# Optimization experiments

Hardware: AMD Instinct MI355X
Metric: run time of the kernel (lower is better)

The kernel has to match this reference:

```python
import jax, jax.numpy as jnp
import numpy as np

DIM = 64
TIME_DIM = 16
LABEL_DIM = 32
N_HEADS = 4
B = 524288


def _mha(seq, w_in, b_in, w_out, b_out, n_heads=N_HEADS):
    # seq: [B, S, E]; faithful nn.MultiheadAttention (batch_first) self-attention
    Bs, S, E = seq.shape
    D = E // n_heads
    qkv = seq @ w_in + b_in  # [B, S, 3E]
    q, k, v = jnp.split(qkv, 3, axis=-1)
    q = q.reshape(Bs, S, n_heads, D)
    k = k.reshape(Bs, S, n_heads, D)
    v = v.reshape(Bs, S, n_heads, D)
    scale = 1.0 / jnp.sqrt(jnp.asarray(D, seq.dtype))
    scores = jnp.einsum('bshd,bthd->bhst', q, k) * scale
    attn = jax.nn.softmax(scores, axis=-1)
    o = jnp.einsum('bhst,bthd->bshd', attn, v).reshape(Bs, S, E)
    return o @ w_out + b_out


def setup_inputs() -> dict:
    key = jax.random.key(0)
    ks = iter(jax.random.split(key, 64))

    def p(shape):
        return jax.random.normal(next(ks), shape, dtype=jnp.float32) * 0.05

    inp = {
        'x': jax.random.normal(next(ks), (B, DIM), dtype=jnp.float32),
        't': jax.random.uniform(next(ks), (B, 1), dtype=jnp.float32),
        'y': jax.random.normal(next(ks), (B, 40), dtype=jnp.float32),
        # label_proj: Linear(40,32) -> ReLU -> Linear(32,64)
        'lp_w1': p((40, LABEL_DIM)), 'lp_b1': p((LABEL_DIM,)),
        'lp_w2': p((LABEL_DIM, DIM)), 'lp_b2': p((DIM,)),
        # two MultiheadAttention layers (packed in_proj, out_proj)
        'a1_win': p((DIM, 3 * DIM)), 'a1_bin': p((3 * DIM,)),
        'a1_wout': p((DIM, DIM)), 'a1_bout': p((DIM,)),
        'a2_win': p((DIM, 3 * DIM)), 'a2_bin': p((3 * DIM,)),
        'a2_wout': p((DIM, DIM)), 'a2_bout': p((DIM,)),
        # FiLM layers: gamma/beta Linear(dim, dim)
        'f1_gw': p((DIM, DIM)), 'f1_gb': p((DIM,)),
        'f1_bw': p((DIM, DIM)), 'f1_bb': p((DIM,)),
        'f2_gw': p((DIM, DIM)), 'f2_gb': p((DIM,)),
        'f2_bw': p((DIM, DIM)), 'f2_bb': p((DIM,)),
        # block1: Linear(80,64)->ReLU->Linear(64,64); block2/3: Linear(64,64)x2
        'b1_w1': p((DIM + TIME_DIM, DIM)), 'b1_b1': p((DIM,)),
        'b1_w2': p((DIM, DIM)), 'b1_b2': p((DIM,)),
        'b2_w1': p((DIM, DIM)), 'b2_b1': p((DIM,)),
        'b2_w2': p((DIM, DIM)), 'b2_b2': p((DIM,)),
        'b3_w1': p((DIM, DIM)), 'b3_b1': p((DIM,)),
        'b3_w2': p((DIM, DIM)), 'b3_b2': p((DIM,)),
        'out_w': p((DIM, DIM)), 'out_b': p((DIM,)),
    }
    return inp


def reference(x, t, y,
              lp_w1, lp_b1, lp_w2, lp_b2,
              a1_win, a1_bin, a1_wout, a1_bout,
              a2_win, a2_bin, a2_wout, a2_bout,
              f1_gw, f1_gb, f1_bw, f1_bb,
              f2_gw, f2_gb, f2_bw, f2_bb,
              b1_w1, b1_b1, b1_w2, b1_b2,
              b2_w1, b2_b1, b2_w2, b2_b2,
              b3_w1, b3_b1, b3_w2, b3_b2,
              out_w, out_b):
    half = TIME_DIM // 2
    freq = (2.0 ** jnp.arange(half, dtype=x.dtype)) * jnp.pi  # [8]
    args = t * freq[None, :]                                   # [B, 8]
    t_feats = jnp.concatenate([jnp.sin(args), jnp.cos(args)], axis=-1)  # [B, 16]

    h = jnp.concatenate([x, t_feats], axis=-1)                 # [B, 80]
    h = jax.nn.relu(h @ b1_w1 + b1_b1) @ b1_w2 + b1_b2         # block1

    y_embed = jax.nn.relu(y @ lp_w1 + lp_b1) @ lp_w2 + lp_b2   # [B, 64]

    seq = jnp.stack([h, y_embed], axis=1)                      # [B, 2, 64]
    h = _mha(seq, a1_win, a1_bin, a1_wout, a1_bout)[:, 0]
    h = (y_embed @ f1_gw + f1_gb) * h + (y_embed @ f1_bw + f1_bb)  # FiLM1
    h = h + (jax.nn.relu(h @ b2_w1 + b2_b1) @ b2_w2 + b2_b2)   # block2 + residual

    seq = jnp.stack([h, y_embed], axis=1)
    h = _mha(seq, a2_win, a2_bin, a2_wout, a2_bout)[:, 0]
    h = (y_embed @ f2_gw + f2_gb) * h + (y_embed @ f2_bw + f2_bb)  # FiLM2
    h = h + (jax.nn.relu(h @ b3_w1 + b3_b1) @ b3_w2 + b3_b2)   # block3 + residual

    return h @ out_w + out_b
```

## Files before the change

kernel.cpp:

```cpp
#include <hip/hip_runtime.h>
#include <math.h>

typedef __attribute__((ext_vector_type(8))) short   short8;
typedef __attribute__((ext_vector_type(8))) _Float16 half8;
typedef __attribute__((ext_vector_type(2))) __fp16  fp16x2;
typedef __attribute__((ext_vector_type(4))) float   f32x4;

__device__ __forceinline__ half8 as_h8(short8 s) {
  union { short8 s; half8 h; } u; u.s = s; return u.h;
}
#define MFMA16(a,b,c) __builtin_amdgcn_mfma_f32_16x16x32_f16(as_h8(a), as_h8(b), (c), 0, 0, 0)

#define WS_B1W1   0
#define WS_B1W2   12
#define WS_LPW1   20
#define WS_LPW2   24
#define WS_A1WIN  28
#define WS_A1WOUT 52
#define WS_F1GW   60
#define WS_F1BW   68
#define WS_B2W1   76
#define WS_B2W2   84
#define WS_A2WIN  92
#define WS_A2WOUT 116
#define WS_F2GW   124
#define WS_F2BW   132
#define WS_B3W1   140
#define WS_B3W2   148
#define WS_OUTW   156
#define WS_FRAGS  164

__device__ __forceinline__ unsigned short f2h(float f) {
  union { _Float16 h; unsigned short u; } r;
  r.h = (_Float16)f;
  return r.u;
}
__device__ __forceinline__ unsigned int pkrtz(float lo, float hi) {
  union { fp16x2 h; unsigned int u; } r;
  r.h = __builtin_amdgcn_cvt_pkrtz(lo, hi);
  return r.u;
}
__device__ __forceinline__ float h_lo(unsigned int p) {
  union { unsigned short s; _Float16 h; } c; c.s = (unsigned short)p; return (float)c.h;
}
__device__ __forceinline__ float h_hi(unsigned int p) {
  union { unsigned short s; _Float16 h; } c; c.s = (unsigned short)(p >> 16); return (float)c.h;
}

__device__ __forceinline__ short8 pack8(float4 a, float4 b) {
  union { unsigned int u[4]; short8 s; } r;
  r.u[0] = pkrtz(a.x, a.y);
  r.u[1] = pkrtz(a.z, a.w);
  r.u[2] = pkrtz(b.x, b.y);
  r.u[3] = pkrtz(b.z, b.w);
  return r.s;
}

__device__ __forceinline__ short8 zero8() {
  short8 r;
  #pragma unroll
  for (int j = 0; j < 8; ++j) r[j] = 0;
  return r;
}

__device__ __forceinline__ short8 neg8(short8 a) {
  union { short8 s; unsigned int u[4]; } r;
  r.s = a;
  #pragma unroll
  for (int i = 0; i < 4; ++i) r.u[i] ^= 0x80008000u;
  return r.s;
}

__device__ __forceinline__ f32x4 relu4(f32x4 v) {
  f32x4 r;
  #pragma unroll
  for (int j = 0; j < 4; ++j) r[j] = fmaxf(v[j], 0.0f);
  return r;
}

__global__ __launch_bounds__(64) void prep_kernel(
    const float* b1w1, const float* b1w2, const float* lpw1, const float* lpw2,
    const float* a1win, const float* a1wout, const float* f1gw, const float* f1bw,
    const float* b2w1, const float* b2w2, const float* a2win, const float* a2wout,
    const float* f2gw, const float* f2bw, const float* b3w1, const float* b3w2,
    const float* outw, unsigned short* ws)
{
  const float* WS_[17] = {b1w1,b1w2,lpw1,lpw2,a1win,a1wout,f1gw,f1bw,b2w1,b2w2,
                          a2win,a2wout,f2gw,f2bw,b3w1,b3w2,outw};
  const int KA[17] = {80,64,40,32,64,64,64,64,64,64,64,64,64,64,64,64,64};
  const int NA[17] = {64,64,32,64,192,64,64,64,64,64,192,64,64,64,64,64,64};
  const int FO[17] = {0,12,20,24,28,52,60,68,76,84,92,116,124,132,140,148,156};

  const int b = blockIdx.x;
  int m = 0;
  #pragma unroll
  for (int i = 1; i < 17; ++i) if (b >= FO[i]) m = i;
  const int f  = b - FO[m];
  const int K  = KA[m], N = NA[m];
  const int kc = (K + 31) >> 5;
  const int n  = f / kc, c = f % kc;

  const int lane = threadIdx.x;
  const int col  = n * 16 + (lane & 15);
  const int kb   = c * 32 + ((lane >> 4) * 8);
  const float* W = WS_[m];

  short8 r;
  #pragma unroll
  for (int j = 0; j < 8; ++j) {
    const int k = kb + j;
    const float v = (k < K) ? W[(size_t)k * N + col] : 0.0f;
    r[j] = (short)f2h(v);
  }
  *reinterpret_cast<short8*>(ws + (size_t)b * 512 + lane * 8) = r;
}

__device__ __forceinline__ short8 ldA(const unsigned short* Ab, int c) {
  return *reinterpret_cast<const short8*>(Ab + c * 32);
}
__device__ __forceinline__ void stC_pk(unsigned short* Cb, int n, unsigned int p01, unsigned int p23) {
  unsigned short* p = Cb + n * 16;
  p[0]   = (unsigned short)p01;
  p[72]  = (unsigned short)(p01 >> 16);
  p[144] = (unsigned short)p23;
  p[216] = (unsigned short)(p23 >> 16);
}
__device__ __forceinline__ void stC(unsigned short* Cb, int n, f32x4 v) {
  stC_pk(Cb, n, pkrtz(v[0], v[1]), pkrtz(v[2], v[3]));
}
__device__ __forceinline__ float rowsum16(float v) {
  float r = v;
  r += __int_as_float(__builtin_amdgcn_update_dpp(
        __float_as_int(r), __float_as_int(r), 0x128, 0xf, 0xf, false));
  r += __int_as_float(__builtin_amdgcn_update_dpp(
        __float_as_int(r), __float_as_int(r), 0x124, 0xf, 0xf, false));
  r += __int_as_float(__builtin_amdgcn_update_dpp(
        __float_as_int(r), __float_as_int(r), 0x122, 0xf, 0xf, false));
  r += __int_as_float(__builtin_amdgcn_update_dpp(
        __float_as_int(r), __float_as_int(r), 0x121, 0xf, 0xf, false));
  return r;
}

__global__ __launch_bounds__(256, 4) void flow_mfma(
    const float* __restrict__ x, const float* __restrict__ t, const float* __restrict__ y,
    const float* __restrict__ b1b1, const float* __restrict__ b1b2,
    const float* __restrict__ lpb1, const float* __restrict__ lpb2,
    const float* __restrict__ a1bin, const float* __restrict__ a1bout,
    const float* __restrict__ f1gb, const float* __restrict__ f1bb,
    const float* __restrict__ b2b1, const float* __restrict__ b2b2,
    const float* __restrict__ a2bin, const float* __restrict__ a2bout,
    const float* __restrict__ f2gb, const float* __restrict__ f2bb,
    const float* __restrict__ b3b1, const float* __restrict__ b3b2,
    const float* __restrict__ outb,
    const unsigned short* __restrict__ ws,
    float* __restrict__ out, int Btotal)
{
  __shared__ __align__(16) unsigned short lds[4][2 * 16 * 72];
  const int tid  = threadIdx.x;
  const int lane = tid & 63, wid = tid >> 6;
  const int lrow = lane & 15, grp = lane >> 4;
  const int r0   = (blockIdx.x * 4 + wid) * 32;
  if (r0 >= Btotal) return;
  unsigned short* T = &lds[wid][0];
  unsigned short* Ab[2];
  unsigned short* Cb[2];
  #pragma unroll
  for (int u = 0; u < 2; ++u) {
    Ab[u] = T + u * 1152 + lrow * 72 + grp * 8;
    Cb[u] = T + u * 1152 + grp * 288 + lrow;
  }
  const short8* wsl = reinterpret_cast<const short8*>(ws) + lane;

  short8 hA0[2], hA1[2];
  {
    short8 tF[2];
    #pragma unroll
    for (int u = 0; u < 2; ++u) {
      const size_t row = (size_t)r0 + u * 16 + lrow;
      const float4* xp = reinterpret_cast<const float4*>(x + row * 64) + grp * 2;
      hA0[u] = pack8(xp[0], xp[1]);
      hA1[u] = pack8(xp[8], xp[9]);
      const float tv = t[row];
      float s = sinf(3.14159265358979323846f * tv);
      float c = cosf(3.14159265358979323846f * tv);
      short8 hp;
      #pragma unroll
      for (int j = 0; j < 8; ++j) {
        const float v = (grp == 0) ? s : ((grp == 1) ? c : 0.0f);
        hp[j] = (short)f2h(v);
        const float s2 = 2.0f * s * c;
        const float c2 = 1.0f - 2.0f * s * s;
        s = s2; c = c2;
      }
      tF[u] = hp;
    }
    #pragma unroll
    for (int n = 0; n < 4; ++n) {
      const short8 B0 = wsl[(WS_B1W1 + n * 3 + 0) * 64];
      const short8 B1 = wsl[(WS_B1W1 + n * 3 + 1) * 64];
      const short8 B2 = wsl[(WS_B1W1 + n * 3 + 2) * 64];
      const float bias = b1b1[n * 16 + lrow];
      #pragma unroll
      for (int u = 0; u < 2; ++u) {
        f32x4 acc = {bias, bias, bias, bias};
        acc = MFMA16(hA0[u], B0, acc);
        acc = MFMA16(hA1[u], B1, acc);
        acc = MFMA16(tF[u],  B2, acc);
        stC(Cb[u], n, relu4(acc));
      }
    }
  }
  #pragma unroll
  for (int u = 0; u < 2; ++u) { hA0[u] = ldA(Ab[u], 0); hA1[u] = ldA(Ab[u], 1); }
  #pragma unroll
  for (int n = 0; n < 4; ++n) {
    const short8 B0 = wsl[(WS_B1W2 + n * 2 + 0) * 64];
    const short8 B1 = wsl[(WS_B1W2 + n * 2 + 1) * 64];
    const float bias = b1b2[n * 16 + lrow];
    #pragma unroll
    for (int u = 0; u < 2; ++u) {
      f32x4 acc = {bias, bias, bias, bias};
      acc = MFMA16(hA0[u], B0, acc);
      acc = MFMA16(hA1[u], B1, acc);
      stC(Cb[u], n, acc);
    }
  }
  #pragma unroll
  for (int u = 0; u < 2; ++u) { hA0[u] = ldA(Ab[u], 0); hA1[u] = ldA(Ab[u], 1); }

  short8 yeA0[2], yeA1[2];
  {
    short8 y0[2], y1[2];
    #pragma unroll
    for (int u = 0; u < 2; ++u) {
      const float* yrow = y + ((size_t)r0 + u * 16 + lrow) * 40;
      y0[u] = pack8(*reinterpret_cast<const float4*>(yrow + grp * 8),
                    *reinterpret_cast<const float4*>(yrow + grp * 8 + 4));
      y1[u] = (grp == 0) ? pack8(*reinterpret_cast<const float4*>(yrow + 32),
                                 *reinterpret_cast<const float4*>(yrow + 36))
                         : zero8();
    }
    #pragma unroll
    for (int n = 0; n < 2; ++n) {
      const short8 B0 = wsl[(WS_LPW1 + n * 2 + 0) * 64];
      const short8 B1 = wsl[(WS_LPW1 + n * 2 + 1) * 64];
      const float bias = lpb1[n * 16 + lrow];
      #pragma unroll
      for (int u = 0; u < 2; ++u) {
        f32x4 acc = {bias, bias, bias, bias};
        acc = MFMA16(y0[u], B0, acc);
        acc = MFMA16(y1[u], B1, acc);
        stC(Cb[u], n, relu4(acc));
      }
    }
    short8 z[2];
    #pragma unroll
    for (int u = 0; u < 2; ++u) z[u] = ldA(Ab[u], 0);
    #pragma unroll
    for (int n = 0; n < 4; ++n) {
      const short8 B0 = wsl[(WS_LPW2 + n) * 64];
      const float bias = lpb2[n * 16 + lrow];
      #pragma unroll
      for (int u = 0; u < 2; ++u)
        stC(Cb[u], n, MFMA16(z[u], B0, ((f32x4){bias, bias, bias, bias})));
    }
    #pragma unroll
    for (int u = 0; u < 2; ++u) { yeA0[u] = ldA(Ab[u], 0); yeA1[u] = ldA(Ab[u], 1); }
  }

  unsigned int hCp01[4][2], hCp23[4][2];
  #pragma unroll 1
  for (int rep = 0; rep < 2; ++rep) {
    const int WIN  = rep ? WS_A2WIN  : WS_A1WIN;
    const int WOUT = rep ? WS_A2WOUT : WS_A1WOUT;
    const int GW   = rep ? WS_F2GW   : WS_F1GW;
    const int BW   = rep ? WS_F2BW   : WS_F1BW;
    const int W1   = rep ? WS_B3W1   : WS_B2W1;
    const int W2   = rep ? WS_B3W2   : WS_B2W2;
    const float* binp  = rep ? a2bin  : a1bin;
    const float* boutp = rep ? a2bout : a1bout;
    const float* gbp   = rep ? f2gb   : f1gb;
    const float* fbp   = rep ? f2bb   : f1bb;
    const float* w1b   = rep ? b3b1   : b2b1;
    const float* w2b   = rep ? b3b2   : b2b2;

    #pragma unroll 1
    for (int n = 0; n < 4; ++n) {
      float pr[2][4];
      {
        const short8 Bq0 = wsl[(WIN + n * 2 + 0) * 64];
        const short8 Bq1 = wsl[(WIN + n * 2 + 1) * 64];
        const short8 Bk0 = wsl[(WIN + (4 + n) * 2 + 0) * 64];
        const short8 Bk1 = wsl[(WIN + (4 + n) * 2 + 1) * 64];
        const float bq = binp[n * 16 + lrow];
        #pragma unroll
        for (int u = 0; u < 2; ++u) {
          f32x4 q = {bq, bq, bq, bq};
          q = MFMA16(hA0[u], Bq0, q);
          q = MFMA16(hA1[u], Bq1, q);
          f32x4 kd = {0.0f, 0.0f, 0.0f, 0.0f};
          kd = MFMA16(hA0[u], Bk0, kd);
          kd = MFMA16(hA1[u], Bk1, kd);
          kd = MFMA16(neg8(yeA0[u]), Bk0, kd);
          kd = MFMA16(neg8(yeA1[u]), Bk1, kd);
          #pragma unroll
          for (int j = 0; j < 4; ++j) {
            const float d = rowsum16(q[j] * kd[j]);
            pr[u][j] = 1.0f / (1.0f + __expf(-0.25f * d));
          }
        }
      }
      {
        const short8 Bv0 = wsl[(WIN + (8 + n) * 2 + 0) * 64];
        const short8 Bv1 = wsl[(WIN + (8 + n) * 2 + 1) * 64];
        const float bv = binp[128 + n * 16 + lrow];
        #pragma unroll
        for (int u = 0; u < 2; ++u) {
          f32x4 v0 = {bv, bv, bv, bv}, v1 = {bv, bv, bv, bv};
          v0 = MFMA16(hA0[u],  Bv0, v0);
          v0 = MFMA16(hA1[u],  Bv1, v0);
          v1 = MFMA16(yeA0[u], Bv0, v1);
          v1 = MFMA16(yeA1[u], Bv1, v1);
          f32x4 ov;
          #pragma unroll
          for (int j = 0; j < 4; ++j) ov[j] = fmaf(pr[u][j], v0[j] - v1[j], v1[j]);
          stC(Cb[u], n, ov);
        }
      }
    }
    #pragma unroll
    for (int u = 0; u < 2; ++u) { hA0[u] = ldA(Ab[u], 0); hA1[u] = ldA(Ab[u], 1); }

    #pragma unroll
    for (int n = 0; n < 4; ++n) {
      f32x4 at[2], g[2];
      {
        const short8 Bo0 = wsl[(WOUT + n * 2 + 0) * 64];
        const short8 Bo1 = wsl[(WOUT + n * 2 + 1) * 64];
        const float bo = boutp[n * 16 + lrow];
        #pragma unroll
        for (int u = 0; u < 2; ++u) {
          at[u] = (f32x4){bo, bo, bo, bo};
          at[u] = MFMA16(hA0[u], Bo0, at[u]);
          at[u] = MFMA16(hA1[u], Bo1, at[u]);
        }
      }
      {
        const short8 Bg0 = wsl[(GW + n * 2 + 0) * 64];
        const short8 Bg1 = wsl[(GW + n * 2 + 1) * 64];
        const float bg = gbp[n * 16 + lrow];
        #pragma unroll
        for (int u = 0; u < 2; ++u) {
          g[u] = (f32x4){bg, bg, bg, bg};
          g[u] = MFMA16(yeA0[u], Bg0, g[u]);
          g[u] = MFMA16(yeA1[u], Bg1, g[u]);
        }
      }
      {
        const short8 Bb0 = wsl[(BW + n * 2 + 0) * 64];
        const short8 Bb1 = wsl[(BW + n * 2 + 1) * 64];
        const float bf = fbp[n * 16 + lrow];
        #pragma unroll
        for (int u = 0; u < 2; ++u) {
          f32x4 fb = {bf, bf, bf, bf};
          fb = MFMA16(yeA0[u], Bb0, fb);
          fb = MFMA16(yeA1[u], Bb1, fb);
          f32x4 hv;
          #pragma unroll
          for (int j = 0; j < 4; ++j) hv[j] = fmaf(g[u][j], at[u][j], fb[j]);
          const unsigned int p01 = pkrtz(hv[0], hv[1]);
          const unsigned int p23 = pkrtz(hv[2], hv[3]);
          hCp01[n][u] = p01; hCp23[n][u] = p23;
          stC_pk(Cb[u], n, p01, p23);
        }
      }
    }
    #pragma unroll
    for (int u = 0; u < 2; ++u) { hA0[u] = ldA(Ab[u], 0); hA1[u] = ldA(Ab[u], 1); }

    #pragma unroll
    for (int n = 0; n < 4; ++n) {
      const short8 B0 = wsl[(W1 + n * 2 + 0) * 64];
      const short8 B1 = wsl[(W1 + n * 2 + 1) * 64];
      const float bias = w1b[n * 16 + lrow];
      #pragma unroll
      for (int u = 0; u < 2; ++u) {
        f32x4 acc = {bias, bias, bias, bias};
        acc = MFMA16(hA0[u], B0, acc);
        acc = MFMA16(hA1[u], B1, acc);
        stC(Cb[u], n, relu4(acc));
      }
    }
    #pragma unroll
    for (int u = 0; u < 2; ++u) { hA0[u] = ldA(Ab[u], 0); hA1[u] = ldA(Ab[u], 1); }
    #pragma unroll
    for (int n = 0; n < 4; ++n) {
      const short8 B0 = wsl[(W2 + n * 2 + 0) * 64];
      const short8 B1 = wsl[(W2 + n * 2 + 1) * 64];
      const float bias = w2b[n * 16 + lrow];
      #pragma unroll
      for (int u = 0; u < 2; ++u) {
        f32x4 acc = {bias, bias, bias, bias};
        acc = MFMA16(hA0[u], B0, acc);
        acc = MFMA16(hA1[u], B1, acc);
        acc[0] += h_lo(hCp01[n][u]);
        acc[1] += h_hi(hCp01[n][u]);
        acc[2] += h_lo(hCp23[n][u]);
        acc[3] += h_hi(hCp23[n][u]);
        stC(Cb[u], n, acc);
      }
    }
    #pragma unroll
    for (int u = 0; u < 2; ++u) { hA0[u] = ldA(Ab[u], 0); hA1[u] = ldA(Ab[u], 1); }
  }

  #pragma unroll 1
  for (int n = 0; n < 4; ++n) {
    const short8 B0 = wsl[(WS_OUTW + n * 2 + 0) * 64];
    const short8 B1 = wsl[(WS_OUTW + n * 2 + 1) * 64];
    const float bias = outb[n * 16 + lrow];
    #pragma unroll
    for (int u = 0; u < 2; ++u) {
      f32x4 a = {bias, bias, bias, bias};
      a = MFMA16(hA0[u], B0, a);
      a = MFMA16(hA1[u], B1, a);
      float* ob = out + ((size_t)r0 + u * 16 + grp * 4) * 64 + n * 16 + lrow;
      #pragma unroll
      for (int j = 0; j < 4; ++j)
        ob[j * 64] = a[j];
    }
  }
}

extern "C" void kernel_launch(void* const* d_in, const int* in_sizes, int n_in,
                              void* d_out, int out_size, void* d_ws, size_t ws_size,
                              hipStream_t stream) {
  (void)n_in; (void)out_size; (void)ws_size;
  const float* p[37];
  for (int i = 0; i < 37; ++i) p[i] = (const float*)d_in[i];
  unsigned short* ws = (unsigned short*)d_ws;

  prep_kernel<<<dim3(WS_FRAGS), dim3(64), 0, stream>>>(
      p[23], p[25], p[3], p[5], p[7], p[9], p[15], p[17],
      p[27], p[29], p[11], p[13], p[19], p[21], p[31], p[33], p[35], ws);

  const int B = in_sizes[0] / 64;
  const int grid = (B + 127) / 128;
  flow_mfma<<<dim3(grid), dim3(256), 0, stream>>>(
      p[0], p[1], p[2],
      p[24], p[26],
      p[4],  p[6],
      p[8],  p[10],
      p[16], p[18],
      p[28], p[30],
      p[12], p[14],
      p[20], p[22],
      p[32], p[34],
      p[36],
      ws, (float*)d_out, B);
}
```

Measured before the change: 191.0 us.

## Fold label projection second layer into downstream attention and FiLM weights

Precomputes products of the label-projection second weight matrix with the key, value, FiLM gamma and FiLM beta weights, plus folded biases, in a new prep kernel. The main kernel then feeds the 32-wide hidden label activation directly into these composed matrices instead of first materializing y_embed. This removes the y_embed GEMM and halves the K-dimension of several MFMAs, and it frees registers. Launch bounds are also raised to 8 blocks per CU for occupancy. Composing the weights in fp32 and rounding once to fp16 changes rounding behaviour slightly.

```diff
diff --git a/kernel.cpp b/kernel.cpp
--- a/kernel.cpp
+++ b/kernel.cpp
@@ -14,21 +14,18 @@
 #define WS_B1W1   0
 #define WS_B1W2   12
 #define WS_LPW1   20
-#define WS_LPW2   24
+#define WS_BIAS   24
 #define WS_A1WIN  28
 #define WS_A1WOUT 52
-#define WS_F1GW   60
-#define WS_F1BW   68
 #define WS_B2W1   76
 #define WS_B2W2   84
 #define WS_A2WIN  92
 #define WS_A2WOUT 116
-#define WS_F2GW   124
-#define WS_F2BW   132
 #define WS_B3W1   140
 #define WS_B3W2   148
 #define WS_OUTW   156
-#define WS_FRAGS  164
+#define WS_COMP   164
+#define WS_FRAGS  196
 
 __device__ __forceinline__ unsigned short f2h(float f) {
   union { _Float16 h; unsigned short u; } r;
@@ -61,14 +58,6 @@
   #pragma unroll
   for (int j = 0; j < 8; ++j) r[j] = 0;
   return r;
-}
-
-__device__ __forceinline__ short8 neg8(short8 a) {
-  union { short8 s; unsigned int u[4]; } r;
-  r.s = a;
-  #pragma unroll
-  for (int i = 0; i < 4; ++i) r.u[i] ^= 0x80008000u;
-  return r.s;
 }
 
 __device__ __forceinline__ f32x4 relu4(f32x4 v) {
@@ -115,6 +104,60 @@
   *reinterpret_cast<short8*>(ws + (size_t)b * 512 + lane * 8) = r;
 }
 
+__global__ __launch_bounds__(64) void prep2_kernel(
+    const float* lpw2, const float* lpb2,
+    const float* a1win, const float* a1bin, const float* a2win, const float* a2bin,
+    const float* f1gw, const float* f1gb, const float* f1bw, const float* f1bb,
+    const float* f2gw, const float* f2gb, const float* f2bw, const float* f2bb,
+    unsigned short* ws)
+{
+  const int b = blockIdx.x, lane = threadIdx.x;
+  if (b < 32) {
+    const int cm = b >> 2, n = b & 3;
+    const float* W; int ldw, colOff; float sgn = 1.0f;
+    switch (cm) {
+      case 0:  W = a1win; ldw = 192; colOff = 64;  sgn = -1.0f; break;
+      case 1:  W = a1win; ldw = 192; colOff = 128; break;
+      case 2:  W = f1gw;  ldw = 64;  colOff = 0;   break;
+      case 3:  W = f1bw;  ldw = 64;  colOff = 0;   break;
+      case 4:  W = a2win; ldw = 192; colOff = 64;  sgn = -1.0f; break;
+      case 5:  W = a2win; ldw = 192; colOff = 128; break;
+      case 6:  W = f2gw;  ldw = 64;  colOff = 0;   break;
+      default: W = f2bw;  ldw = 64;  colOff = 0;   break;
+    }
+    const int col = colOff + n * 16 + (lane & 15);
+    const int kb  = (lane >> 4) * 8;
+    short8 r;
+    #pragma unroll
+    for (int j = 0; j < 8; ++j) {
+      const int k = kb + j;
+      float acc = 0.0f;
+      for (int m = 0; m < 64; ++m) acc += lpw2[k * 64 + m] * W[(size_t)m * ldw + col];
+      r[j] = (short)f2h(sgn * acc);
+    }
+    *reinterpret_cast<short8*>(ws + (size_t)(WS_COMP + b) * 512 + lane * 8) = r;
+  } else {
+    const int vb = b - 32;
+    const int rep = vb >> 2, which = vb & 3;
+    const float* win = rep ? a2win : a1win;
+    const float* bin = rep ? a2bin : a1bin;
+    const float* W; int ldw, colOff; const float* bias0 = nullptr; float sgn = 1.0f;
+    switch (which) {
+      case 0:  W = win; ldw = 192; colOff = 64;  sgn = -1.0f; break;
+      case 1:  W = win; ldw = 192; colOff = 128; bias0 = bin + 128; break;
+      case 2:  W = rep ? f2gw : f1gw; ldw = 64; colOff = 0; bias0 = rep ? f2gb : f1gb; break;
+      default: W = rep ? f2bw : f1bw; ldw = 64; colOff = 0; bias0 = rep ? f2bb : f1bb; break;
+    }
+    const int c = lane;
+    float acc = 0.0f;
+    for (int m = 0; m < 64; ++m) acc += lpb2[m] * W[(size_t)m * ldw + colOff + c];
+    acc *= sgn;
+    if (bias0) acc += bias0[c];
+    float* wsb = reinterpret_cast<float*>(ws + WS_BIAS * 512);
+    wsb[rep * 256 + which * 64 + c] = acc;
+  }
+}
+
 __device__ __forceinline__ short8 ldA(const unsigned short* Ab, int c) {
   return *reinterpret_cast<const short8*>(Ab + c * 32);
 }
@@ -141,15 +184,13 @@
   return r;
 }
 
-__global__ __launch_bounds__(256, 4) void flow_mfma(
+__global__ __launch_bounds__(256, 8) void flow_mfma(
     const float* __restrict__ x, const float* __restrict__ t, const float* __restrict__ y,
     const float* __restrict__ b1b1, const float* __restrict__ b1b2,
-    const float* __restrict__ lpb1, const float* __restrict__ lpb2,
+    const float* __restrict__ lpb1,
     const float* __restrict__ a1bin, const float* __restrict__ a1bout,
-    const float* __restrict__ f1gb, const float* __restrict__ f1bb,
+    const float* __restrict__ a2bin, const float* __restrict__ a2bout,
     const float* __restrict__ b2b1, const float* __restrict__ b2b2,
-    const float* __restrict__ a2bin, const float* __restrict__ a2bout,
-    const float* __restrict__ f2gb, const float* __restrict__ f2bb,
     const float* __restrict__ b3b1, const float* __restrict__ b3b2,
     const float* __restrict__ outb,
     const unsigned short* __restrict__ ws,
@@ -170,6 +211,7 @@
     Cb[u] = T + u * 1152 + grp * 288 + lrow;
   }
   const short8* wsl = reinterpret_cast<const short8*>(ws) + lane;
+  const float*  wsb = reinterpret_cast<const float*>(ws + WS_BIAS * 512);
 
   short8 hA0[2], hA1[2];
   {
@@ -228,7 +270,7 @@
   #pragma unroll
   for (int u = 0; u < 2; ++u) { hA0[u] = ldA(Ab[u], 0); hA1[u] = ldA(Ab[u], 1); }
 
-  short8 yeA0[2], yeA1[2];
+  short8 zA[2];
   {
     short8 y0[2], y1[2];
     #pragma unroll
@@ -253,19 +295,8 @@
         stC(Cb[u], n, relu4(acc));
       }
     }
-    short8 z[2];
-    #pragma unroll
-    for (int u = 0; u < 2; ++u) z[u] = ldA(Ab[u], 0);
-    #pragma unroll
-    for (int n = 0; n < 4; ++n) {
-      const short8 B0 = wsl[(WS_LPW2 + n) * 64];
-      const float bias = lpb2[n * 16 + lrow];
-      #pragma unroll
-      for (int u = 0; u < 2; ++u)
-        stC(Cb[u], n, MFMA16(z[u], B0, ((f32x4){bias, bias, bias, bias})));
-    }
-    #pragma unroll
-    for (int u = 0; u < 2; ++u) { yeA0[u] = ldA(Ab[u], 0); yeA1[u] = ldA(Ab[u], 1); }
+    #pragma unroll
+    for (int u = 0; u < 2; ++u) zA[u] = ldA(Ab[u], 0);
   }
 
   unsigned int hCp01[4][2], hCp23[4][2];
@@ -273,16 +304,17 @@
   for (int rep = 0; rep < 2; ++rep) {
     const int WIN  = rep ? WS_A2WIN  : WS_A1WIN;
     const int WOUT = rep ? WS_A2WOUT : WS_A1WOUT;
-    const int GW   = rep ? WS_F2GW   : WS_F1GW;
-    const int BW   = rep ? WS_F2BW   : WS_F1BW;
+    const int CK   = WS_COMP + rep * 16;
+    const int CV   = WS_COMP + rep * 16 + 4;
+    const int CG   = WS_COMP + rep * 16 + 8;
+    const int CB   = WS_COMP + rep * 16 + 12;
     const int W1   = rep ? WS_B3W1   : WS_B2W1;
     const int W2   = rep ? WS_B3W2   : WS_B2W2;
     const float* binp  = rep ? a2bin  : a1bin;
     const float* boutp = rep ? a2bout : a1bout;
-    const float* gbp   = rep ? f2gb   : f1gb;
-    const float* fbp   = rep ? f2bb   : f1bb;
     const float* w1b   = rep ? b3b1   : b2b1;
     const float* w2b   = rep ? b3b2   : b2b2;
+    const float* bcomp = wsb + rep * 256;
 
     #pragma unroll 1
     for (int n = 0; n < 4; ++n) {
@@ -292,17 +324,18 @@
         const short8 Bq1 = wsl[(WIN + n * 2 + 1) * 64];
         const short8 Bk0 = wsl[(WIN + (4 + n) * 2 + 0) * 64];
         const short8 Bk1 = wsl[(WIN + (4 + n) * 2 + 1) * 64];
+        const short8 BCK = wsl[(CK + n) * 64];
         const float bq = binp[n * 16 + lrow];
+        const float ck = bcomp[n * 16 + lrow];
         #pragma unroll
         for (int u = 0; u < 2; ++u) {
           f32x4 q = {bq, bq, bq, bq};
           q = MFMA16(hA0[u], Bq0, q);
           q = MFMA16(hA1[u], Bq1, q);
-          f32x4 kd = {0.0f, 0.0f, 0.0f, 0.0f};
+          f32x4 kd = {ck, ck, ck, ck};
           kd = MFMA16(hA0[u], Bk0, kd);
           kd = MFMA16(hA1[u], Bk1, kd);
-          kd = MFMA16(neg8(yeA0[u]), Bk0, kd);
-          kd = MFMA16(neg8(yeA1[u]), Bk1, kd);
+          kd = MFMA16(zA[u],  BCK, kd);
           #pragma unroll
           for (int j = 0; j < 4; ++j) {
             const float d = rowsum16(q[j] * kd[j]);
@@ -313,14 +346,16 @@
       {
         const short8 Bv0 = wsl[(WIN + (8 + n) * 2 + 0) * 64];
         const short8 Bv1 = wsl[(WIN + (8 + n) * 2 + 1) * 64];
-        const float bv = binp[128 + n * 16 + lrow];
+        const short8 BCV = wsl[(CV + n) * 64];
+        const float bv  = binp[128 + n * 16 + lrow];
+        const float bvp = bcomp[64 + n * 16 + lrow];
         #pragma unroll
         for (int u = 0; u < 2; ++u) {
-          f32x4 v0 = {bv, bv, bv, bv}, v1 = {bv, bv, bv, bv};
-          v0 = MFMA16(hA0[u],  Bv0, v0);
-          v0 = MFMA16(hA1[u],  Bv1, v0);
-          v1 = MFMA16(yeA0[u], Bv0, v1);
-          v1 = MFMA16(yeA1[u], Bv1, v1);
+          f32x4 v0 = {bv, bv, bv, bv};
+          v0 = MFMA16(hA0[u], Bv0, v0);
+          v0 = MFMA16(hA1[u], Bv1, v0);
+          f32x4 v1 = {bvp, bvp, bvp, bvp};
+          v1 = MFMA16(zA[u], BCV, v1);
           f32x4 ov;
           #pragma unroll
           for (int j = 0; j < 4; ++j) ov[j] = fmaf(pr[u][j], v0[j] - v1[j], v1[j]);
@@ -333,7 +368,7 @@
 
     #pragma unroll
     for (int n = 0; n < 4; ++n) {
-      f32x4 at[2], g[2];
+      f32x4 at[2];
       {
         const short8 Bo0 = wsl[(WOUT + n * 2 + 0) * 64];
         const short8 Bo1 = wsl[(WOUT + n * 2 + 1) * 64];
@@ -346,28 +381,19 @@
         }
       }
       {
-        const short8 Bg0 = wsl[(GW + n * 2 + 0) * 64];
-        const short8 Bg1 = wsl[(GW + n * 2 + 1) * 64];
-        const float bg = gbp[n * 16 + lrow];
+        const short8 BG = wsl[(CG + n) * 64];
+        const short8 BB = wsl[(CB + n) * 64];
+        const float gp  = bcomp[128 + n * 16 + lrow];
+        const float fbp = bcomp[192 + n * 16 + lrow];
         #pragma unroll
         for (int u = 0; u < 2; ++u) {
-          g[u] = (f32x4){bg, bg, bg, bg};
-          g[u] = MFMA16(yeA0[u], Bg0, g[u]);
-          g[u] = MFMA16(yeA1[u], Bg1, g[u]);
-        }
-      }
-      {
-        const short8 Bb0 = wsl[(BW + n * 2 + 0) * 64];
-        const short8 Bb1 = wsl[(BW + n * 2 + 1) * 64];
-        const float bf = fbp[n * 16 + lrow];
-        #pragma unroll
-        for (int u = 0; u < 2; ++u) {
-          f32x4 fb = {bf, bf, bf, bf};
-          fb = MFMA16(yeA0[u], Bb0, fb);
-          fb = MFMA16(yeA1[u], Bb1, fb);
+          f32x4 g = {gp, gp, gp, gp};
+          g = MFMA16(zA[u], BG, g);
+          f32x4 fb = {fbp, fbp, fbp, fbp};
+          fb = MFMA16(zA[u], BB, fb);
           f32x4 hv;
           #pragma unroll
-          for (int j = 0; j < 4; ++j) hv[j] = fmaf(g[u][j], at[u][j], fb[j]);
+          for (int j = 0; j < 4; ++j) hv[j] = fmaf(g[j], at[u][j], fb[j]);
           const unsigned int p01 = pkrtz(hv[0], hv[1]);
           const unsigned int p23 = pkrtz(hv[2], hv[3]);
           hCp01[n][u] = p01; hCp23[n][u] = p23;
@@ -440,21 +466,26 @@
   for (int i = 0; i < 37; ++i) p[i] = (const float*)d_in[i];
   unsigned short* ws = (unsigned short*)d_ws;
 
-  prep_kernel<<<dim3(WS_FRAGS), dim3(64), 0, stream>>>(
+  prep_kernel<<<dim3(164), dim3(64), 0, stream>>>(
       p[23], p[25], p[3], p[5], p[7], p[9], p[15], p[17],
       p[27], p[29], p[11], p[13], p[19], p[21], p[31], p[33], p[35], ws);
+
+  prep2_kernel<<<dim3(40), dim3(64), 0, stream>>>(
+      p[5],  p[6],
+      p[7],  p[8],  p[11], p[12],
+      p[15], p[16], p[17], p[18],
+      p[19], p[20], p[21], p[22],
+      ws);
 
   const int B = in_sizes[0] / 64;
   const int grid = (B + 127) / 128;
   flow_mfma<<<dim3(grid), dim3(256), 0, stream>>>(
       p[0], p[1], p[2],
       p[24], p[26],
-      p[4],  p[6],
+      p[4],
       p[8],  p[10],
-      p[16], p[18],
+      p[12], p[14],
       p[28], p[30],
-      p[12], p[14],
-      p[20], p[22],
       p[32], p[34],
       p[36],
       ws, (float*)d_out, B);
```

Result: slower. 370.8 us (+94.1%).
